# Performance work log

Measured on AMD Instinct MI355X. Metric: run time of the kernel, lower is better.

The kernel has to match this reference:

```python
import jax, jax.numpy as jnp
import numpy as np

N, E, B, K = 100000, 3200000, 500, 30
F_IN, H1, NUM_CLASSES = 128, 64, 18


def _gcn_conv(x, W, b, row, col, w_edge, n_nodes):
    # PyG GCNConv: remove_self_loops happened outside (w_edge=0 on self loops),
    # GCNConv re-adds self loops -> deg = in_deg + 1, norm = d^-1/2[row]*d^-1/2[col].
    xw = x @ W
    deg = jax.ops.segment_sum(w_edge, col, num_segments=n_nodes) + 1.0
    dis = jax.lax.rsqrt(deg)
    coef = dis[row] * dis[col] * w_edge           # [E]
    msg = xw[row] * coef[:, None]                 # [E, C] irregular gather
    agg = jax.ops.segment_sum(msg, col, num_segments=n_nodes)
    agg = agg + xw * (dis * dis)[:, None]         # self-loop term
    return agg + b


def _sort_pool(x, batch, num_graphs, k):
    # SortAggregation: per-graph sort descending by last channel, keep top-k, zero-pad.
    n, c = x.shape
    score = x[:, -1]
    perm = jnp.lexsort((-score, batch))           # sort by (batch asc, score desc)
    b_sorted = batch[perm]
    counts = jax.ops.segment_sum(jnp.ones((n,), x.dtype), batch, num_segments=num_graphs)
    starts = jnp.cumsum(counts) - counts          # segment start offsets
    pos = jnp.arange(n) - starts[b_sorted].astype(jnp.int32)
    pos = jnp.where(pos < k, pos, k)              # out-of-range -> dropped
    out = jnp.zeros((num_graphs, k, c), x.dtype).at[b_sorted, pos].set(x[perm], mode='drop')
    return out.reshape(num_graphs, k * c)


def _conv1d(x, w, b, stride):
    y = jax.lax.conv_general_dilated(x, w, (stride,), 'VALID',
                                     dimension_numbers=('NCH', 'OIH', 'NCH'))
    return y + b[None, :, None]


def setup_inputs() -> dict:
    key = jax.random.key(0)
    ks = jax.random.split(key, 16)
    x = jax.random.normal(ks[0], (N, F_IN), dtype=jnp.float32)
    edge_index = jax.random.randint(ks[1], (2, E), 0, N, dtype=jnp.int32)
    batch = jnp.sort(jax.random.randint(ks[2], (N,), 0, B, dtype=jnp.int32))
    s = 0.05
    return {
        'x': x, 'edge_index': edge_index, 'batch': batch, 'num_graphs': B,
        'W1': jax.random.normal(ks[3], (F_IN, H1), jnp.float32) * s,
        'b1': jnp.zeros((H1,), jnp.float32),
        'W2': jax.random.normal(ks[4], (H1, 1), jnp.float32) * s,
        'b2': jnp.zeros((1,), jnp.float32),
        'conv3_w': jax.random.normal(ks[5], (16, 1, 97), jnp.float32) * s,
        'conv3_b': jnp.zeros((16,), jnp.float32),
        'conv4_w': jax.random.normal(ks[6], (32, 16, 5), jnp.float32) * s,
        'conv4_b': jnp.zeros((32,), jnp.float32),
        'fc1_w': jax.random.normal(ks[7], (192, 128), jnp.float32) * s,
        'fc1_b': jnp.zeros((128,), jnp.float32),
        'fc2_w': jax.random.normal(ks[8], (128, NUM_CLASSES), jnp.float32) * s,
        'fc2_b': jnp.zeros((NUM_CLASSES,), jnp.float32),
    }


def reference(x, edge_index, batch, num_graphs, W1, b1, W2, b2,
              conv3_w, conv3_b, conv4_w, conv4_b, fc1_w, fc1_b, fc2_w, fc2_b):
    row, col = edge_index[0], edge_index[1]
    w_edge = (row != col).astype(x.dtype)         # remove_self_loops
    x1 = jnp.tanh(_gcn_conv(x, W1, b1, row, col, w_edge, x.shape[0]))   # [N,64]
    x2 = jnp.tanh(_gcn_conv(x1, W2, b2, row, col, w_edge, x.shape[0]))  # [N,1]
    xc = jnp.concatenate([x1, x2], axis=-1)       # [N,65]
    p = _sort_pool(xc, batch, num_graphs, K)      # [B, 1950]
    h = p[:, None, :]                             # [B,1,1950]
    h = jax.nn.relu(_conv1d(h, conv3_w, conv3_b, 97))                   # [B,16,20]
    h = jax.lax.reduce_window(h, -jnp.inf, jax.lax.max,
                              (1, 1, 2), (1, 1, 2), 'VALID')            # [B,16,10]
    h = jax.nn.relu(_conv1d(h, conv4_w, conv4_b, 1))                    # [B,32,6]
    h = h.reshape(h.shape[0], -1)                 # [B,192]
    last_layer = jax.nn.relu(h @ fc1_w + fc1_b)   # [B,128] (dropout = eval identity)
    out = last_layer @ fc2_w + fc2_b              # [B,18]
    classes = jax.nn.log_softmax(out, axis=-1)
    return (classes, out, last_layer)
```

## Files before the change

### kernel.cpp

```cpp
#include <hip/hip_runtime.h>
#include <math.h>

#define N_NODES 100000
#define N_EDGES 3200000
#define B_GRAPHS 500
#define K_TOP 30
#define F_INN 128
#define H1C 64
#define NUM_CLASSES 18
#define XC 65
#define P_LEN (K_TOP * XC)
#define C3_OUT 16
#define C3_K 97
#define C3_L 20
#define P2_L 10
#define C4_OUT 32
#define C4_K 5
#define C4_L 6
#define FC1_IN 192
#define FC1_OUT 128

#define BK_SHIFT 7
#define BK_NODES 128
#define NBKT ((N_NODES + BK_NODES - 1) / BK_NODES)
#define BSTRIDE 5120
#define MS_EPT 32
#define MS_EPB (256 * MS_EPT)

#define REG_B 544

typedef __attribute__((ext_vector_type(8))) short bf16x8;
typedef __attribute__((ext_vector_type(4))) float f32x4;
typedef __attribute__((ext_vector_type(2))) unsigned int u32x2;

static __device__ __forceinline__ unsigned short f2bf(float f) {
    unsigned int u = __float_as_uint(f);
    u += 0x7FFFu + ((u >> 16) & 1u);
    return (unsigned short)(u >> 16);
}

__global__ __launch_bounds__(256) void k_mscatter(const int* __restrict__ row,
                                                  const int* __restrict__ col,
                                                  int* __restrict__ gcur,
                                                  unsigned int* __restrict__ ebkt) {
    __shared__ int hist[NBKT];
    __shared__ int base[NBKT];
    int tid = threadIdx.x;
    for (int i = tid; i < NBKT; i += 256) hist[i] = 0;
    __syncthreads();
    unsigned int pk[MS_EPT];
    unsigned int pay[MS_EPT];
    int e0q = blockIdx.x * (MS_EPB / 4);
#pragma unroll
    for (int j = 0; j < MS_EPT / 4; ++j) {
        int q = e0q + j * 256 + tid;
        bool ok = (q * 4) < N_EDGES;
        int4 r4 = ok ? ((const int4*)row)[q] : make_int4(0, 0, 0, 0);
        int4 c4 = ok ? ((const int4*)col)[q] : make_int4(0, 0, 0, 0);
#pragma unroll
        for (int k = 0; k < 4; ++k) {
            int jj = j * 4 + k;
            pk[jj] = 0xFFFFFFFFu;
            int r = k == 0 ? r4.x : k == 1 ? r4.y : k == 2 ? r4.z : r4.w;
            int c = k == 0 ? c4.x : k == 1 ? c4.y : k == 2 ? c4.z : c4.w;
            if (ok && r != c) {
                int b = c >> BK_SHIFT;
                int rank = atomicAdd(&hist[b], 1);
                pk[jj] = ((unsigned int)b << 12) | (unsigned int)rank;
                pay[jj] = ((unsigned int)r << BK_SHIFT) | (unsigned int)(c & (BK_NODES - 1));
            }
        }
    }
    __syncthreads();
    for (int i = tid; i < NBKT; i += 256)
        base[i] = hist[i] ? (i * BSTRIDE + atomicAdd(&gcur[i], hist[i])) : 0;
    __syncthreads();
#pragma unroll
    for (int j = 0; j < MS_EPT; ++j) {
        if (pk[j] != 0xFFFFFFFFu) {
            int b = pk[j] >> 12;
            int rank = pk[j] & 0xFFF;
            ebkt[base[b] + rank] = pay[j];
        }
    }
}

__global__ __launch_bounds__(256) void k_csr(const unsigned int* __restrict__ ebkt,
                                             const int* __restrict__ gcur,
                                             float* __restrict__ dis,
                                             int2* __restrict__ rowse,
                                             int* __restrict__ erow) {
    __shared__ unsigned int ebs[BSTRIDE];
    __shared__ int cnt[BK_NODES];
    __shared__ int s[256];
    __shared__ int cur[BK_NODES];
    int b = blockIdx.x, t = threadIdx.x;
    if (t < BK_NODES) cnt[t] = 0;
    __syncthreads();
    int n = gcur[b];
    int lo = b * BSTRIDE;
    for (int i = t; i < n; i += 256) {
        unsigned int pk = ebkt[lo + i];
        ebs[i] = pk;
        atomicAdd(&cnt[pk & (BK_NODES - 1)], 1);
    }
    __syncthreads();
    int v = (t < BK_NODES) ? cnt[t] : 0;
    s[t] = v;
    __syncthreads();
    for (int off = 1; off < BK_NODES; off <<= 1) {
        int add = (t >= off) ? s[t - off] : 0;
        __syncthreads();
        s[t] += add;
        __syncthreads();
    }
    int ex = s[t] - v;
    if (t < BK_NODES) {
        int node = b * BK_NODES + t;
        if (node < N_NODES) {
            dis[node] = rsqrtf((float)v + 1.0f);
            rowse[node] = make_int2(lo + ex, lo + ex + v);
        }
        cur[t] = lo + ex;
    }
    __syncthreads();
    for (int i = t; i < n; i += 256) {
        unsigned int pk = ebs[i];
        int cl = pk & (BK_NODES - 1);
        int slot = atomicAdd(&cur[cl], 1);
        erow[slot] = (int)((pk >> BK_SHIFT) << 7);
    }
}

__global__ __launch_bounds__(256) void k_xw1(const float* __restrict__ x,
                                             const float* __restrict__ W1,
                                             const float* __restrict__ dis,
                                             unsigned short* __restrict__ xw) {
    __shared__ unsigned short w1s[16 * 64 * 8];
    int tid = threadIdx.x;
    if (blockIdx.x == 0 && tid < 32)
        ((unsigned int*)(xw + (size_t)N_NODES * H1C))[tid] = 0;
    for (int idx = tid; idx < 16 * 64 * 8; idx += 256) {
        int f = idx >> 9;
        int l = (idx >> 3) & 63;
        int j = idx & 7;
        int kq = f >> 2, t4 = f & 3;
        int k = kq * 32 + ((l >> 4) << 3) + j;
        int n = t4 * 16 + (l & 15);
        w1s[idx] = f2bf(W1[k * H1C + n]);
    }
    __syncthreads();
    int wave = tid >> 6;
    int lane = tid & 63;
    int quad = lane >> 4;
    int m = lane & 15;
    int wrow0 = blockIdx.x * 64 + wave * 16;

    bf16x8 bw[16];
#pragma unroll
    for (int f = 0; f < 16; ++f)
        bw[f] = *(const bf16x8*)&w1s[(f * 64 + lane) * 8];

    f32x4 acc[4];
#pragma unroll
    for (int t = 0; t < 4; ++t) acc[t] = (f32x4){0.f, 0.f, 0.f, 0.f};

    int rowA = wrow0 + m;
    size_t ra = (size_t)(rowA < N_NODES ? rowA : N_NODES - 1);
#pragma unroll
    for (int kq = 0; kq < 4; ++kq) {
        const float* xp = x + ra * F_INN + kq * 32 + quad * 8;
        float4 f0 = ((const float4*)xp)[0];
        float4 f1 = ((const float4*)xp)[1];
        bf16x8 a;
        a[0] = (short)f2bf(f0.x); a[1] = (short)f2bf(f0.y);
        a[2] = (short)f2bf(f0.z); a[3] = (short)f2bf(f0.w);
        a[4] = (short)f2bf(f1.x); a[5] = (short)f2bf(f1.y);
        a[6] = (short)f2bf(f1.z); a[7] = (short)f2bf(f1.w);
#pragma unroll
        for (int t = 0; t < 4; ++t)
            acc[t] = __builtin_amdgcn_mfma_f32_16x16x32_bf16(a, bw[kq * 4 + t], acc[t], 0, 0, 0);
    }
#pragma unroll
    for (int r = 0; r < 4; ++r) {
        int rowD = wrow0 + quad * 4 + r;
        if (rowD < N_NODES) {
            float dsc = dis[rowD];
#pragma unroll
            for (int t = 0; t < 4; ++t)
                xw[(size_t)rowD * H1C + t * 16 + m] = f2bf(acc[t][r] * dsc);
        }
    }
}

__global__ __launch_bounds__(256) void k_agg1m(const int2* __restrict__ rowse,
                                               const int* __restrict__ erow,
                                               const unsigned short* __restrict__ xws,
                                               const float* __restrict__ dis,
                                               const float* __restrict__ b1,
                                               const float* __restrict__ W2,
                                               float* __restrict__ x1,
                                               float* __restrict__ xws2) {
    __shared__ __align__(16) char slds[4][8 * REG_B];
    int tid = threadIdx.x;
    int wave = tid >> 6;
    int lane = tid & 63;
    int wid = blockIdx.x * 4 + wave;
    int grp = lane >> 3;
    int sub = lane & 7;
    int2 se = rowse[wid];
    int base = se.x, endp = se.y;
    int nE = endp - base;
    const char* xb = (const char*)xws;
    const int ZR = N_NODES << 7;

    char* wreg = &slds[wave][0];
    char* dst0 = wreg + ((sub >> 1) * 2 + ((grp >> 2) & 1)) * REG_B + (grp & 3) * 32 + (sub & 1) * 16;
    unsigned int trb = (unsigned int)(size_t)wreg +
                       (unsigned int)(((lane >> 4) * 64 + (lane & 15)) * 2);

    bf16x8 aones;
#pragma unroll
    for (int i = 0; i < 8; ++i) aones[i] = (short)0x3F80;

    f32x4 ac0 = (f32x4){0.f, 0.f, 0.f, 0.f};
    f32x4 ac1 = ac0, ac2 = ac0, ac3 = ac0;

    int nGroups = (nE + 63) >> 6;
    int mo = ((base + lane) < endp) ? erow[base + lane] : ZR;
    uint4 v0, v1, v2, v3;
    if (nE > 0) {
        int o0 = __shfl(mo, grp);
        int o1 = __shfl(mo, 8 + grp);
        int o2 = __shfl(mo, 16 + grp);
        int o3 = __shfl(mo, 24 + grp);
        v0 = ((const uint4*)(xb + o0))[sub];
        v1 = ((const uint4*)(xb + o1))[sub];
        v2 = ((const uint4*)(xb + o2))[sub];
        v3 = ((const uint4*)(xb + o3))[sub];
    }
    for (int g = 0; g < nGroups; ++g) {
        int idxn = base + (g + 1) * 64 + lane;
        int mo_next = (idxn < endp) ? erow[idxn] : ZR;
#pragma unroll
        for (int hf = 0; hf < 2; ++hf) {
            int hw = g * 2 + hf;
            if (hw * 32 < nE) {
                *(uint4*)(dst0)       = v0;
                *(uint4*)(dst0 + 128) = v1;
                *(uint4*)(dst0 + 256) = v2;
                *(uint4*)(dst0 + 384) = v3;
                int nhw = hw + 1;
                if (nhw * 32 < nE) {
                    int moS = (nhw & 1) ? mo : mo_next;
                    int off = (nhw & 1) << 5;
                    int o0 = __shfl(moS, off + grp);
                    int o1 = __shfl(moS, off + 8 + grp);
                    int o2 = __shfl(moS, off + 16 + grp);
                    int o3 = __shfl(moS, off + 24 + grp);
                    v0 = ((const uint4*)(xb + o0))[sub];
                    v1 = ((const uint4*)(xb + o1))[sub];
                    v2 = ((const uint4*)(xb + o2))[sub];
                    v3 = ((const uint4*)(xb + o3))[sub];
                }
                asm volatile("s_waitcnt lgkmcnt(0)" ::: "memory");
                __builtin_amdgcn_sched_barrier(0);
                u32x2 q0, q1, q2, q3, q4, q5, q6, q7;
                asm volatile("ds_read_b64_tr_b16 %0, %1 offset:0"    : "=v"(q0) : "v"(trb) : "memory");
                asm volatile("ds_read_b64_tr_b16 %0, %1 offset:544"  : "=v"(q1) : "v"(trb) : "memory");
                asm volatile("ds_read_b64_tr_b16 %0, %1 offset:1088" : "=v"(q2) : "v"(trb) : "memory");
                asm volatile("ds_read_b64_tr_b16 %0, %1 offset:1632" : "=v"(q3) : "v"(trb) : "memory");
                asm volatile("ds_read_b64_tr_b16 %0, %1 offset:2176" : "=v"(q4) : "v"(trb) : "memory");
                asm volatile("ds_read_b64_tr_b16 %0, %1 offset:2720" : "=v"(q5) : "v"(trb) : "memory");
                asm volatile("ds_read_b64_tr_b16 %0, %1 offset:3264" : "=v"(q6) : "v"(trb) : "memory");
                asm volatile("ds_read_b64_tr_b16 %0, %1 offset:3808" : "=v"(q7) : "v"(trb) : "memory");
                asm volatile("s_waitcnt lgkmcnt(0)" ::: "memory");
                __builtin_amdgcn_sched_barrier(0);
                union FU { bf16x8 f; unsigned int d[4]; };
                FU f0, f1, f2, f3;
                f0.d[0] = q0.x; f0.d[1] = q0.y; f0.d[2] = q1.x; f0.d[3] = q1.y;
                f1.d[0] = q2.x; f1.d[1] = q2.y; f1.d[2] = q3.x; f1.d[3] = q3.y;
                f2.d[0] = q4.x; f2.d[1] = q4.y; f2.d[2] = q5.x; f2.d[3] = q5.y;
                f3.d[0] = q6.x; f3.d[1] = q6.y; f3.d[2] = q7.x; f3.d[3] = q7.y;
                ac0 = __builtin_amdgcn_mfma_f32_16x16x32_bf16(aones, f0.f, ac0, 0, 0, 0);
                ac1 = __builtin_amdgcn_mfma_f32_16x16x32_bf16(aones, f1.f, ac1, 0, 0, 0);
                ac2 = __builtin_amdgcn_mfma_f32_16x16x32_bf16(aones, f2.f, ac2, 0, 0, 0);
                ac3 = __builtin_amdgcn_mfma_f32_16x16x32_bf16(aones, f3.f, ac3, 0, 0, 0);
            }
        }
        mo = mo_next;
    }
    float v0s = __shfl(ac0[0], lane & 15);
    float v1s = __shfl(ac1[0], lane & 15);
    float v2s = __shfl(ac2[0], lane & 15);
    float v3s = __shfl(ac3[0], lane & 15);
    int ts = lane >> 4;
    float aggv = ts == 0 ? v0s : (ts == 1 ? v1s : (ts == 2 ? v2s : v3s));
    float d = dis[wid];
    unsigned int su = xws[(size_t)wid * H1C + lane];
    float self = __uint_as_float(su << 16);
    float v = tanhf(d * (aggv + self) + b1[lane]);
    x1[(size_t)wid * H1C + lane] = v;
    float s = v * W2[lane];
#pragma unroll
    for (int off = 1; off < 64; off <<= 1) s += __shfl_xor(s, off);
    if (lane == 0) xws2[wid] = d * s;
}

__global__ __launch_bounds__(256) void k_x2(const int2* __restrict__ rowse,
                                            const int* __restrict__ erow,
                                            const float* __restrict__ xws2,
                                            const float* __restrict__ dis,
                                            const float* __restrict__ b2,
                                            float* __restrict__ x2) {
    int lane = threadIdx.x & 63;
    int wglob = (blockIdx.x * 256 + threadIdx.x) >> 6;
    int grp = lane >> 3;
    int sub = lane & 7;
    int node = wglob * 8 + grp;
    int2 se = rowse[node];
    float acc = 0.0f;
    for (int i = se.x + sub; i < se.y; i += 8)
        acc += xws2[erow[i] >> 7];
    acc += __shfl_xor(acc, 1);
    acc += __shfl_xor(acc, 2);
    acc += __shfl_xor(acc, 4);
    if (sub == 0)
        x2[node] = tanhf(dis[node] * (acc + xws2[node]) + b2[0]);
}

__global__ __launch_bounds__(256) void k_poolhead(const int* __restrict__ batch,
                                                  const float* __restrict__ x1,
                                                  const float* __restrict__ x2,
                                                  const float* __restrict__ w3, const float* __restrict__ b3,
                                                  const float* __restrict__ w4, const float* __restrict__ b4,
                                                  const float* __restrict__ fw1, const float* __restrict__ fb1,
                                                  const float* __restrict__ fw2, const float* __restrict__ fb2,
                                                  float* __restrict__ out) {
    __shared__ float x2s[512];
    __shared__ int sel[K_TOP];
    __shared__ float ps[P_LEN];
    __shared__ float h1s[C3_OUT * C3_L];
    __shared__ float h2s[C3_OUT * P2_L];
    __shared__ float h3s[FC1_IN];
    __shared__ float lls[FC1_OUT];
    __shared__ float outs[NUM_CLASSES];
    int g = blockIdx.x, tid = threadIdx.x;
    int lo = 0, hi = N_NODES;
    while (lo < hi) { int m = (lo + hi) >> 1; if (batch[m] < g) lo = m + 1; else hi = m; }
    int start = lo;
    hi = N_NODES;
    while (lo < hi) { int m = (lo + hi) >> 1; if (batch[m] < g + 1) lo = m + 1; else hi = m; }
    int end = lo;
    int count = end - start;
    if (count > 512) count = 512;
    for (int t = tid; t < count; t += 256) x2s[t] = x2[start + t];
    __syncthreads();
    int wave = tid >> 6, lane = tid & 63;
    if (wave == 0) {
        unsigned long long k[8];
#pragma unroll
        for (int i = 0; i < 8; ++i) {
            int idx = i * 64 + lane;
            unsigned long long key = 0ULL;
            if (idx < count) {
                unsigned int bits = __float_as_uint(x2s[idx]);
                unsigned int u = (bits & 0x80000000u) ? ~bits : (bits | 0x80000000u);
                key = ((unsigned long long)u << 32) | (unsigned int)(~(unsigned int)(start + idx));
            }
            k[i] = key;
        }
        int kk = count < K_TOP ? count : K_TOP;
        for (int j = 0; j < kk; ++j) {
            unsigned long long best = k[0];
#pragma unroll
            for (int i = 1; i < 8; ++i) if (k[i] > best) best = k[i];
#pragma unroll
            for (int off = 32; off; off >>= 1) {
                unsigned long long o = __shfl_xor(best, off);
                if (o > best) best = o;
            }
            int node = (int)(~(unsigned int)(best & 0xFFFFFFFFULL));
#pragma unroll
            for (int i = 0; i < 8; ++i) if (k[i] == best) k[i] = 0ULL;
            if (lane == 0) sel[j] = node;
        }
        if (lane >= kk && lane < K_TOP) sel[lane] = -1;
    }
    __syncthreads();
    for (int t = tid; t < P_LEN; t += 256) {
        int j = t / XC, c = t - j * XC;
        int node = sel[j];
        float v = 0.0f;
        if (node >= 0) v = (c < H1C) ? x1[(size_t)node * H1C + c] : x2s[node - start];
        ps[t] = v;
    }
    __syncthreads();
    for (int o = tid; o < C3_OUT * C3_L; o += 256) {
        int oc = o / C3_L, pos = o % C3_L;
        float s = b3[oc];
        const float* w = w3 + oc * C3_K;
        int base = pos * C3_K;
        for (int k = 0; k < C3_K; ++k) s += ps[base + k] * w[k];
        h1s[o] = fmaxf(s, 0.0f);
    }
    __syncthreads();
    if (tid < C3_OUT * P2_L) {
        int oc = tid / P2_L, pos = tid % P2_L;
        h2s[tid] = fmaxf(h1s[oc * C3_L + 2 * pos], h1s[oc * C3_L + 2 * pos + 1]);
    }
    __syncthreads();
    if (tid < C4_OUT * C4_L) {
        int oc = tid / C4_L, pos = tid % C4_L;
        float s = b4[oc];
        for (int ic = 0; ic < C3_OUT; ++ic)
#pragma unroll
            for (int k = 0; k < C4_K; ++k)
                s += h2s[ic * P2_L + pos + k] * w4[oc * C3_OUT * C4_K + ic * C4_K + k];
        h3s[oc * C4_L + pos] = fmaxf(s, 0.0f);
    }
    __syncthreads();
    if (tid < FC1_OUT) {
        float s = fb1[tid];
        for (int i = 0; i < FC1_IN; ++i) s += h3s[i] * fw1[i * FC1_OUT + tid];
        float v = fmaxf(s, 0.0f);
        lls[tid] = v;
        out[2 * B_GRAPHS * NUM_CLASSES + (size_t)g * FC1_OUT + tid] = v;
    }
    __syncthreads();
    if (tid < NUM_CLASSES) {
        float s = fb2[tid];
        for (int j = 0; j < FC1_OUT; ++j) s += lls[j] * fw2[j * NUM_CLASSES + tid];
        outs[tid] = s;
        out[B_GRAPHS * NUM_CLASSES + (size_t)g * NUM_CLASSES + tid] = s;
    }
    __syncthreads();
    if (tid < NUM_CLASSES) {
        float m = -INFINITY;
        for (int k2 = 0; k2 < NUM_CLASSES; ++k2) m = fmaxf(m, outs[k2]);
        float se = 0.0f;
        for (int k2 = 0; k2 < NUM_CLASSES; ++k2) se += expf(outs[k2] - m);
        out[(size_t)g * NUM_CLASSES + tid] = outs[tid] - m - logf(se);
    }
}

extern "C" void kernel_launch(void* const* d_in, const int* in_sizes, int n_in,
                              void* d_out, int out_size, void* d_ws, size_t ws_size,
                              hipStream_t stream) {
    const float* x   = (const float*)d_in[0];
    const int*   ei  = (const int*)d_in[1];
    const int*   row = ei;
    const int*   col = ei + N_EDGES;
    const int*   bat = (const int*)d_in[2];
    const float* W1  = (const float*)d_in[4];
    const float* b1  = (const float*)d_in[5];
    const float* W2  = (const float*)d_in[6];
    const float* b2  = (const float*)d_in[7];
    const float* w3  = (const float*)d_in[8];
    const float* b3  = (const float*)d_in[9];
    const float* w4  = (const float*)d_in[10];
    const float* b4  = (const float*)d_in[11];
    const float* fw1 = (const float*)d_in[12];
    const float* fb1 = (const float*)d_in[13];
    const float* fw2 = (const float*)d_in[14];
    const float* fb2 = (const float*)d_in[15];

    char* wsb = (char*)d_ws;
    unsigned short* xws = (unsigned short*)wsb;       wsb += (size_t)(N_NODES + 1) * H1C * 2;
    float* x1     = (float*)wsb;                      wsb += (size_t)N_NODES * H1C * 4;
    int*   erow   = (int*)wsb;                        wsb += (size_t)NBKT * BSTRIDE * 4;
    unsigned int* ebkt = (unsigned int*)x1;
    int*   gcur   = (int*)wsb;                        wsb += (size_t)NBKT * 4;
    int2*  rowse  = (int2*)wsb;                       wsb += (size_t)N_NODES * 8;
    float* dis    = (float*)wsb;                      wsb += (size_t)N_NODES * 4;
    float* xws2   = (float*)wsb;                      wsb += (size_t)N_NODES * 4;
    float* x2     = (float*)wsb;                      wsb += (size_t)N_NODES * 4;
    float* outp   = (float*)d_out;

    hipMemsetAsync(gcur, 0, (size_t)NBKT * 4, stream);

    k_mscatter<<<(N_EDGES + MS_EPB - 1) / MS_EPB, 256, 0, stream>>>(row, col, gcur, ebkt);
    k_csr<<<NBKT, 256, 0, stream>>>(ebkt, gcur, dis, rowse, erow);
    k_xw1<<<(N_NODES + 63) / 64, 256, 0, stream>>>(x, W1, dis, xws);
    k_agg1m<<<N_NODES / 4, 256, 0, stream>>>(rowse, erow, xws, dis, b1, W2, x1, xws2);
    k_x2<<<N_NODES / (8 * 4), 256, 0, stream>>>(rowse, erow, xws2, dis, b2, x2);
    k_poolhead<<<B_GRAPHS, 256, 0, stream>>>(bat, x1, x2,
                                             w3, b3, w4, b4, fw1, fb1, fw2, fb2, outp);
}
```

Baseline: 314.6 us.

## Fuse second GCN layer aggregation into pool-head kernel and drop gather prefetch

The second-layer GCN aggregation (x2) is now computed per graph inside the sort-pool/head kernel instead of a separate kernel, removing a launch and the x2 round-trip through global memory. Separately, the first-layer aggregation loop drops its register double-buffered prefetch of neighbor rows and instead loads and stores each group directly before the LDS transpose/MFMA step. The fusion lowers parallelism for the x2 gather to 500 blocks, and removing the prefetch reduces register use but exposes gather latency.

```diff
diff --git a/kernel.cpp b/kernel.cpp
--- a/kernel.cpp
+++ b/kernel.cpp
@@ -226,42 +226,17 @@
     f32x4 ac0 = (f32x4){0.f, 0.f, 0.f, 0.f};
     f32x4 ac1 = ac0, ac2 = ac0, ac3 = ac0;
 
-    int nGroups = (nE + 63) >> 6;
-    int mo = ((base + lane) < endp) ? erow[base + lane] : ZR;
-    uint4 v0, v1, v2, v3;
-    if (nE > 0) {
-        int o0 = __shfl(mo, grp);
-        int o1 = __shfl(mo, 8 + grp);
-        int o2 = __shfl(mo, 16 + grp);
-        int o3 = __shfl(mo, 24 + grp);
-        v0 = ((const uint4*)(xb + o0))[sub];
-        v1 = ((const uint4*)(xb + o1))[sub];
-        v2 = ((const uint4*)(xb + o2))[sub];
-        v3 = ((const uint4*)(xb + o3))[sub];
-    }
-    for (int g = 0; g < nGroups; ++g) {
-        int idxn = base + (g + 1) * 64 + lane;
-        int mo_next = (idxn < endp) ? erow[idxn] : ZR;
+    for (int w0 = 0; w0 < nE; w0 += 64) {
+        int idx = base + w0 + lane;
+        int myoff = (idx < endp) ? erow[idx] : ZR;
 #pragma unroll
         for (int hf = 0; hf < 2; ++hf) {
-            int hw = g * 2 + hf;
-            if (hw * 32 < nE) {
-                *(uint4*)(dst0)       = v0;
-                *(uint4*)(dst0 + 128) = v1;
-                *(uint4*)(dst0 + 256) = v2;
-                *(uint4*)(dst0 + 384) = v3;
-                int nhw = hw + 1;
-                if (nhw * 32 < nE) {
-                    int moS = (nhw & 1) ? mo : mo_next;
-                    int off = (nhw & 1) << 5;
-                    int o0 = __shfl(moS, off + grp);
-                    int o1 = __shfl(moS, off + 8 + grp);
-                    int o2 = __shfl(moS, off + 16 + grp);
-                    int o3 = __shfl(moS, off + 24 + grp);
-                    v0 = ((const uint4*)(xb + o0))[sub];
-                    v1 = ((const uint4*)(xb + o1))[sub];
-                    v2 = ((const uint4*)(xb + o2))[sub];
-                    v3 = ((const uint4*)(xb + o3))[sub];
+            if (w0 + hf * 32 < nE) {
+#pragma unroll
+                for (int ii = 0; ii < 4; ++ii) {
+                    int o = __shfl(myoff, hf * 32 + ii * 8 + grp);
+                    uint4 v = ((const uint4*)(xb + o))[sub];
+                    *(uint4*)(dst0 + ii * 128) = v;
                 }
                 asm volatile("s_waitcnt lgkmcnt(0)" ::: "memory");
                 __builtin_amdgcn_sched_barrier(0);
@@ -288,7 +263,6 @@
                 ac3 = __builtin_amdgcn_mfma_f32_16x16x32_bf16(aones, f3.f, ac3, 0, 0, 0);
             }
         }
-        mo = mo_next;
     }
     float v0s = __shfl(ac0[0], lane & 15);
     float v1s = __shfl(ac1[0], lane & 15);
@@ -307,31 +281,13 @@
     if (lane == 0) xws2[wid] = d * s;
 }
 
-__global__ __launch_bounds__(256) void k_x2(const int2* __restrict__ rowse,
-                                            const int* __restrict__ erow,
-                                            const float* __restrict__ xws2,
-                                            const float* __restrict__ dis,
-                                            const float* __restrict__ b2,
-                                            float* __restrict__ x2) {
-    int lane = threadIdx.x & 63;
-    int wglob = (blockIdx.x * 256 + threadIdx.x) >> 6;
-    int grp = lane >> 3;
-    int sub = lane & 7;
-    int node = wglob * 8 + grp;
-    int2 se = rowse[node];
-    float acc = 0.0f;
-    for (int i = se.x + sub; i < se.y; i += 8)
-        acc += xws2[erow[i] >> 7];
-    acc += __shfl_xor(acc, 1);
-    acc += __shfl_xor(acc, 2);
-    acc += __shfl_xor(acc, 4);
-    if (sub == 0)
-        x2[node] = tanhf(dis[node] * (acc + xws2[node]) + b2[0]);
-}
-
 __global__ __launch_bounds__(256) void k_poolhead(const int* __restrict__ batch,
                                                   const float* __restrict__ x1,
-                                                  const float* __restrict__ x2,
+                                                  const int2* __restrict__ rowse,
+                                                  const int* __restrict__ erow,
+                                                  const float* __restrict__ xws2,
+                                                  const float* __restrict__ dis,
+                                                  const float* __restrict__ b2,
                                                   const float* __restrict__ w3, const float* __restrict__ b3,
                                                   const float* __restrict__ w4, const float* __restrict__ b4,
                                                   const float* __restrict__ fw1, const float* __restrict__ fb1,
@@ -354,9 +310,27 @@
     int end = lo;
     int count = end - start;
     if (count > 512) count = 512;
-    for (int t = tid; t < count; t += 256) x2s[t] = x2[start + t];
-    __syncthreads();
     int wave = tid >> 6, lane = tid & 63;
+    {
+        float b2v = b2[0];
+        int grp8 = lane >> 3, sub8 = lane & 7;
+        for (int t0 = 0; t0 < count; t0 += 32) {
+            int li = t0 + wave * 8 + grp8;
+            float acc = 0.0f;
+            int node = start + li;
+            if (li < count) {
+                int2 se = rowse[node];
+                for (int i = se.x + sub8; i < se.y; i += 8)
+                    acc += xws2[erow[i] >> 7];
+            }
+            acc += __shfl_xor(acc, 1);
+            acc += __shfl_xor(acc, 2);
+            acc += __shfl_xor(acc, 4);
+            if (li < count && sub8 == 0)
+                x2s[li] = tanhf(dis[node] * (acc + xws2[node]) + b2v);
+        }
+    }
+    __syncthreads();
     if (wave == 0) {
         unsigned long long k[8];
 #pragma unroll
@@ -474,7 +448,6 @@
     int2*  rowse  = (int2*)wsb;                       wsb += (size_t)N_NODES * 8;
     float* dis    = (float*)wsb;                      wsb += (size_t)N_NODES * 4;
     float* xws2   = (float*)wsb;                      wsb += (size_t)N_NODES * 4;
-    float* x2     = (float*)wsb;                      wsb += (size_t)N_NODES * 4;
     float* outp   = (float*)d_out;
 
     hipMemsetAsync(gcur, 0, (size_t)NBKT * 4, stream);
@@ -483,7 +456,6 @@
     k_csr<<<NBKT, 256, 0, stream>>>(ebkt, gcur, dis, rowse, erow);
     k_xw1<<<(N_NODES + 63) / 64, 256, 0, stream>>>(x, W1, dis, xws);
     k_agg1m<<<N_NODES / 4, 256, 0, stream>>>(rowse, erow, xws, dis, b1, W2, x1, xws2);
-    k_x2<<<N_NODES / (8 * 4), 256, 0, stream>>>(rowse, erow, xws2, dis, b2, x2);
-    k_poolhead<<<B_GRAPHS, 256, 0, stream>>>(bat, x1, x2,
+    k_poolhead<<<B_GRAPHS, 256, 0, stream>>>(bat, x1, rowse, erow, xws2, dis, b2,
                                              w3, b3, w4, b4, fw1, fb1, fw2, fb2, outp);
 }
```

Measured after the change: 311.8 us. Within noise of the previous version (-0.9%).
